# Optimization experiments

Measured on AMD Instinct MI355X. Metric: run time of the kernel, lower is better.

## Reference

```python
import jax, jax.numpy as jnp
import numpy as np

B, L, D, H = 2, 2048, 1024, 16
DH = D // H  # 64


def setup_inputs() -> dict:
    key = jax.random.key(0)
    ks = jax.random.split(key, 11)
    s = 0.02
    return {
        "src": jax.random.normal(ks[0], (B, L, D), dtype=jnp.float32),
        "Wq": jax.random.normal(ks[1], (D, D), dtype=jnp.float32) * s,
        "bq": jax.random.normal(ks[2], (D,), dtype=jnp.float32) * s,
        "Wk": jax.random.normal(ks[3], (D, D), dtype=jnp.float32) * s,
        "bk": jax.random.normal(ks[4], (D,), dtype=jnp.float32) * s,
        "Wv": jax.random.normal(ks[5], (D, D), dtype=jnp.float32) * s,
        "bv": jax.random.normal(ks[6], (D,), dtype=jnp.float32) * s,
        "Wo": jax.random.normal(ks[7], (D, D), dtype=jnp.float32) * s,
        "bo": jax.random.normal(ks[8], (D,), dtype=jnp.float32) * s,
        "conv_w": jax.random.normal(ks[9], (H, D, 3), dtype=jnp.float32) * s,  # Conv1d weight [out=H, in=D, k=3]
        "conv_b": jax.random.normal(ks[10], (H,), dtype=jnp.float32) * s,
    }


def reference(src, Wq, bq, Wk, bk, Wv, bv, Wo, bo, conv_w, conv_b):
    b, l, d = src.shape
    h, dh = H, DH
    # QKV projections (torch Linear: x @ W.T + b), split into heads: [B,H,L,DH]
    Q = (src @ Wq.T + bq).reshape(b, l, h, dh).transpose(0, 2, 1, 3)
    K = (src @ Wk.T + bk).reshape(b, l, h, dh).transpose(0, 2, 1, 3)
    V = (src @ Wv.T + bv).reshape(b, l, h, dh).transpose(0, 2, 1, 3)
    # saliency conv: Conv1d(D->H, k=3, padding='same') on [B,D,L] -> [B,H,L]
    sal = jax.lax.conv_general_dilated(
        src.transpose(0, 2, 1), conv_w,
        window_strides=(1,), padding=[(1, 1)],
        dimension_numbers=("NCH", "OIH", "NCH"),
    ) + conv_b[None, :, None]
    # attention scores + per-head saliency bias (broadcast over query axis)
    scores = jnp.einsum("bhqd,bhkd->bhqk", Q, K) / jnp.sqrt(jnp.float32(dh))
    scores = scores + sal[:, :, None, :]
    attn = jax.nn.softmax(scores, axis=-1)  # dropout is identity in eval
    out = jnp.einsum("bhqk,bhkd->bhqd", attn, V)  # [B,H,L,DH]
    out = out.transpose(0, 2, 1, 3).reshape(b, l, d)
    out = out @ Wo.T + bo
    return out, attn
```

## Files before the change

### kernel.cpp

```cpp
#include <hip/hip_runtime.h>

typedef __bf16 bf16x8 __attribute__((ext_vector_type(8)));
typedef float f32x4 __attribute__((ext_vector_type(4)));
typedef unsigned short u16;
typedef unsigned int u32;

#define MFMA(a, b, c) __builtin_amdgcn_mfma_f32_16x16x32_bf16((a), (b), (c), 0, 0, 0)


__device__ __forceinline__ u16 f2bf(float f) {
  u32 u = __float_as_uint(f);
  return (u16)((u + 0x7fffu + ((u >> 16) & 1u)) >> 16);
}

__global__ __launch_bounds__(256) void prep_all(
    const float4* __restrict__ src, const float4* __restrict__ wq,
    const float4* __restrict__ wk, const float4* __restrict__ wv,
    const float4* __restrict__ wo, const float* __restrict__ cw,
    uint2* __restrict__ srcb, uint2* __restrict__ wqb, uint2* __restrict__ wkb,
    uint2* __restrict__ wvb, uint2* __restrict__ wob, float* __restrict__ cwT) {
  int bx = blockIdx.x;
  if (bx < 8192) {
    const float4* in;
    uint2* out;
    int base;
    if (bx < 4096) { in = src; out = srcb; base = 0; }
    else if (bx < 5120) { in = wq; out = wqb; base = 4096; }
    else if (bx < 6144) { in = wk; out = wkb; base = 5120; }
    else if (bx < 7168) { in = wv; out = wvb; base = 6144; }
    else { in = wo; out = wob; base = 7168; }
    int i = (bx - base) * 256 + threadIdx.x;
    float4 v = in[i];
    uint2 o;
    o.x = (u32)f2bf(v.x) | ((u32)f2bf(v.y) << 16);
    o.y = (u32)f2bf(v.z) | ((u32)f2bf(v.w) << 16);
    out[i] = o;
  } else {
    int i = (bx - 8192) * 256 + threadIdx.x;
    int h = i / 3072;
    int j = (i - h * 3072) >> 10;
    int d = i & 1023;
    cwT[i] = cw[(h * 1024 + d) * 3 + j];
  }
}

__global__ __launch_bounds__(256) void conv_sal_k(const float* __restrict__ src,
                                                  const float* __restrict__ cwT,
                                                  const float* __restrict__ cb,
                                                  float* __restrict__ sal) {
  __shared__ float part[4][16][17];
  const int t = threadIdx.x;
  const int h = t & 15;
  const int li = (t >> 4) & 3;
  const int dc = t >> 6;
  const int b = blockIdx.y;
  const int l = blockIdx.x * 4 + li;
  float4 acc = {0.f, 0.f, 0.f, 0.f};
#pragma unroll
  for (int j = 0; j < 3; j++) {
    int ls = l + j - 1;
    if (ls < 0 || ls >= 2048) continue;
    const float4* sp = (const float4*)(src + ((size_t)b * 2048 + ls) * 1024 + dc * 256);
    const float4* wp = (const float4*)(cwT + (h * 3 + j) * 1024 + dc * 256);
    for (int d = 0; d < 64; d++) {
      float4 a = sp[d], w = wp[d];
      acc.x += a.x * w.x;
      acc.y += a.y * w.y;
      acc.z += a.z * w.z;
      acc.w += a.w * w.w;
    }
  }
  part[dc][li][h] = (acc.x + acc.y) + (acc.z + acc.w);
  __syncthreads();
  if (dc == 0) {
    float s = cb[h] + ((part[0][li][h] + part[1][li][h]) + (part[2][li][h] + part[3][li][h]));
    sal[(b * 16 + h) * 2048 + l] = s;
  }
}

__device__ __forceinline__ void gemm_core(const u16* __restrict__ Xg, const u16* __restrict__ Wg,
                                          int mblk, int nblk, u16* smA, u16* smB,
                                          f32x4 acc[4][4]) {
  const int t = threadIdx.x;
  const int lane = t & 63, wid = t >> 6;
  const int cl = lane & 15, gp = lane >> 4;
  const int r0 = t >> 2, cc = (t & 3) * 8;
  const u16* gA0 = Xg + (size_t)(mblk + r0) * 1024 + cc;
  const u16* gB0 = Wg + (size_t)(nblk + r0) * 1024 + cc;
  u16* lA0 = smA + t * 8;
  u16* lB0 = smB + t * 8;
  const u16* rA = smA + ((wid >> 1) * 64 + cl) * 32 + gp * 8;
  const u16* rB = smB + ((wid & 1) * 64 + cl) * 32 + gp * 8;
  for (int k0 = 0; k0 < 1024; k0 += 32) {
    bf16x8 sa0 = *(const bf16x8*)(gA0 + k0);
    bf16x8 sa1 = *(const bf16x8*)(gA0 + 64 * 1024 + k0);
    bf16x8 sb0 = *(const bf16x8*)(gB0 + k0);
    bf16x8 sb1 = *(const bf16x8*)(gB0 + 64 * 1024 + k0);
    __syncthreads();
    *(bf16x8*)lA0 = sa0;
    *(bf16x8*)(lA0 + 2048) = sa1;
    *(bf16x8*)lB0 = sb0;
    *(bf16x8*)(lB0 + 2048) = sb1;
    __syncthreads();
    bf16x8 a[4], b[4];
#pragma unroll
    for (int i = 0; i < 4; i++) {
      a[i] = *(const bf16x8*)(rA + i * 512);
      b[i] = *(const bf16x8*)(rB + i * 512);
    }
#pragma unroll
    for (int tm = 0; tm < 4; tm++)
#pragma unroll
      for (int tn = 0; tn < 4; tn++) acc[tm][tn] = MFMA(a[tm], b[tn], acc[tm][tn]);
  }
}

__global__ __launch_bounds__(256) void qkv_gemm(
    const u16* __restrict__ Xb, const u16* __restrict__ Wqb, const u16* __restrict__ Wkb,
    const u16* __restrict__ Wvb, const float* __restrict__ bq, const float* __restrict__ bk,
    const float* __restrict__ bv, u16* __restrict__ Qb, u16* __restrict__ Kb,
    u16* __restrict__ Vt) {
  __shared__ __align__(16) u16 smA[4096], smB[4096];
  const int seg = blockIdx.x >> 3;
  const u16* __restrict__ W = (seg == 0) ? Wqb : (seg == 1) ? Wkb : Wvb;
  const float* __restrict__ bias = (seg == 0) ? bq : (seg == 1) ? bk : bv;
  const int lane = threadIdx.x & 63, wid = threadIdx.x >> 6;
  const int cl = lane & 15, gp = lane >> 4;
  const int mblk = blockIdx.y * 128, nblk = (blockIdx.x & 7) * 128;
  const int m0 = mblk + (wid >> 1) * 64;
  const int n0 = nblk + (wid & 1) * 64;
  f32x4 acc[4][4] = {};
  gemm_core(Xb, W, mblk, nblk, smA, smB, acc);
#pragma unroll
  for (int tn = 0; tn < 4; tn++) {
    int col = n0 + tn * 16 + cl;
    float bv_ = bias[col];
    int hh = col >> 6, dh = col & 63;
#pragma unroll
    for (int tm = 0; tm < 4; tm++) {
#pragma unroll
      for (int r = 0; r < 4; r++) {
        int row = m0 + tm * 16 + gp * 4 + r;
        u16 hv = f2bf(acc[tm][tn][r] + bv_);
        int bb = row >> 11, l = row & 2047;
        if (seg == 0)
          Qb[(((size_t)(bb * 16 + hh) * 2048 + l) << 6) + dh] = hv;
        else if (seg == 1)
          Kb[(((size_t)(bb * 16 + hh) * 2048 + l) << 6) + dh] = hv;
        else
          Vt[((size_t)(bb * 16 + hh) * 64 + dh) * 2048 + l] = hv;
      }
    }
  }
}

__global__ __launch_bounds__(256) void out_gemm(const u16* __restrict__ Xb,
                                                const u16* __restrict__ W,
                                                const float* __restrict__ bias,
                                                float* __restrict__ Y) {
  __shared__ __align__(16) u16 smA[4096], smB[4096];
  const int lane = threadIdx.x & 63, wid = threadIdx.x >> 6;
  const int cl = lane & 15, gp = lane >> 4;
  const int mblk = blockIdx.y * 128, nblk = blockIdx.x * 128;
  const int m0 = mblk + (wid >> 1) * 64;
  const int n0 = nblk + (wid & 1) * 64;
  f32x4 acc[4][4] = {};
  gemm_core(Xb, W, mblk, nblk, smA, smB, acc);
#pragma unroll
  for (int tn = 0; tn < 4; tn++) {
    int col = n0 + tn * 16 + cl;
    float bv_ = bias[col];
#pragma unroll
    for (int tm = 0; tm < 4; tm++)
#pragma unroll
      for (int r = 0; r < 4; r++) {
        int row = m0 + tm * 16 + gp * 4 + r;
        Y[(size_t)row * 1024 + col] = acc[tm][tn][r] + bv_;
      }
  }
}

__global__ __launch_bounds__(128, 6) void flash_fused(const u16* __restrict__ Qb,
                                                      const u16* __restrict__ Kb,
                                                      const u16* __restrict__ Vt,
                                                      const float* __restrict__ sal,
                                                      float* __restrict__ attn,
                                                      u16* __restrict__ Ob) {
  __shared__ __align__(16) u16 pbuf[2][16][72];
  const int bh = blockIdx.x;
  const int b = bh >> 4, h = bh & 15;
  const int lane = threadIdx.x & 63, wid = threadIdx.x >> 6;
  const int cl = lane & 15, gp = lane >> 4;
  const int q0 = blockIdx.y * 32 + wid * 16;
  const u16* Qh = Qb + (size_t)bh * 2048 * 64;
  const u16* Kh = Kb + (size_t)bh * 2048 * 64;
  const u16* Vh = Vt + (size_t)bh * 64 * 2048;
  const float* salh = sal + bh * 2048;
  bf16x8 aQ0 = *(const bf16x8*)(Qh + (size_t)(q0 + cl) * 64 + gp * 8);
  bf16x8 aQ1 = *(const bf16x8*)(Qh + (size_t)(q0 + cl) * 64 + 32 + gp * 8);

  float ml[4], ll[4];
#pragma unroll
  for (int r = 0; r < 4; r++) { ml[r] = -1e30f; ll[r] = 0.f; }
  for (int kb = 0; kb < 2048; kb += 64) {
    f32x4 st[4];
#pragma unroll
    for (int tn = 0; tn < 4; tn++) {
      const u16* kp = Kh + (size_t)(kb + tn * 16 + cl) * 64 + gp * 8;
      f32x4 s = {};
      s = MFMA(aQ0, *(const bf16x8*)kp, s);
      s = MFMA(aQ1, *(const bf16x8*)(kp + 32), s);
      st[tn] = s;
    }
#pragma unroll
    for (int tn = 0; tn < 4; tn++) {
      float sv = salh[kb + tn * 16 + cl];
#pragma unroll
      for (int r = 0; r < 4; r++) st[tn][r] = st[tn][r] * 0.125f + sv;
    }
#pragma unroll
    for (int r = 0; r < 4; r++) {
      float v = fmaxf(fmaxf(st[0][r], st[1][r]), fmaxf(st[2][r], st[3][r]));
      float mn = fmaxf(ml[r], v);
      float alpha = __expf(ml[r] - mn);
      ml[r] = mn;
      float s0 = __expf(st[0][r] - mn) + __expf(st[1][r] - mn) + __expf(st[2][r] - mn) +
                 __expf(st[3][r] - mn);
      ll[r] = ll[r] * alpha + s0;
    }
  }
  float m[4], il[4];
#pragma unroll
  for (int r = 0; r < 4; r++) {
    float mr = ml[r];
    mr = fmaxf(mr, __shfl_xor(mr, 1));
    mr = fmaxf(mr, __shfl_xor(mr, 2));
    mr = fmaxf(mr, __shfl_xor(mr, 4));
    mr = fmaxf(mr, __shfl_xor(mr, 8));
    float lr = ll[r] * __expf(ml[r] - mr);
    lr += __shfl_xor(lr, 1);
    lr += __shfl_xor(lr, 2);
    lr += __shfl_xor(lr, 4);
    lr += __shfl_xor(lr, 8);
    m[r] = mr;
    il[r] = 1.0f / lr;
  }

  f32x4 oacc[4] = {};
  float* arow = attn + (size_t)bh * 2048 * 2048;
  u16* pw = &pbuf[wid][0][0];
  for (int kb = 0; kb < 2048; kb += 64) {
    f32x4 st[4];
#pragma unroll
    for (int tn = 0; tn < 4; tn++) {
      const u16* kp = Kh + (size_t)(kb + tn * 16 + cl) * 64 + gp * 8;
      f32x4 s = {};
      s = MFMA(aQ0, *(const bf16x8*)kp, s);
      s = MFMA(aQ1, *(const bf16x8*)(kp + 32), s);
      st[tn] = s;
    }
#pragma unroll
    for (int tn = 0; tn < 4; tn++) {
      float sv = salh[kb + tn * 16 + cl];
#pragma unroll
      for (int r = 0; r < 4; r++) {
        float p = __expf(st[tn][r] * 0.125f + sv - m[r]);
        arow[(size_t)(q0 + gp * 4 + r) * 2048 + kb + tn * 16 + cl] = p * il[r];
        pw[(gp * 4 + r) * 72 + tn * 16 + cl] = f2bf(p);
      }
    }
    asm volatile("s_waitcnt lgkmcnt(0)" ::: "memory");
    __builtin_amdgcn_sched_barrier(0);
    bf16x8 aP0 = *(const bf16x8*)(pw + cl * 72 + gp * 8);
    bf16x8 aP1 = *(const bf16x8*)(pw + cl * 72 + 32 + gp * 8);
    asm volatile("" ::: "memory");
#pragma unroll
    for (int tn = 0; tn < 4; tn++) {
      const u16* vp = Vh + (size_t)(tn * 16 + cl) * 2048 + kb + gp * 8;
      oacc[tn] = MFMA(aP0, *(const bf16x8*)vp, oacc[tn]);
      oacc[tn] = MFMA(aP1, *(const bf16x8*)(vp + 32), oacc[tn]);
    }
  }
#pragma unroll
  for (int tn = 0; tn < 4; tn++) {
    int d = h * 64 + tn * 16 + cl;
#pragma unroll
    for (int r = 0; r < 4; r++) {
      int q = q0 + gp * 4 + r;
      Ob[((size_t)(b * 2048 + q)) * 1024 + d] = f2bf(oacc[tn][r] * il[r]);
    }
  }
}

extern "C" void kernel_launch(void* const* d_in, const int* in_sizes, int n_in,
                              void* d_out, int out_size, void* d_ws, size_t ws_size,
                              hipStream_t stream) {
  const float* src = (const float*)d_in[0];
  const float* Wq = (const float*)d_in[1];
  const float* bq = (const float*)d_in[2];
  const float* Wk = (const float*)d_in[3];
  const float* bk = (const float*)d_in[4];
  const float* Wv = (const float*)d_in[5];
  const float* bv = (const float*)d_in[6];
  const float* Wo = (const float*)d_in[7];
  const float* bo = (const float*)d_in[8];
  const float* cw = (const float*)d_in[9];
  const float* cb = (const float*)d_in[10];

  char* ws = (char*)d_ws;
  u16* srcb = (u16*)(ws + 0);
  u16* wqb = (u16*)(ws + 8388608);
  u16* wkb = (u16*)(ws + 10485760);
  u16* wvb = (u16*)(ws + 12582912);
  u16* wob = (u16*)(ws + 14680064);
  u16* Qb = (u16*)(ws + 16777216);
  u16* Kb = (u16*)(ws + 25165824);
  u16* Vt = (u16*)(ws + 33554432);
  u16* Ob = (u16*)(ws + 41943040);
  float* cwT = (float*)(ws + 50331648);
  float* sal = (float*)(ws + 50528256);

  float* outp = (float*)d_out;
  float* attn = (float*)d_out + 4194304;

  prep_all<<<8384, 256, 0, stream>>>((const float4*)src, (const float4*)Wq, (const float4*)Wk,
                                     (const float4*)Wv, (const float4*)Wo, cw,
                                     (uint2*)srcb, (uint2*)wqb, (uint2*)wkb, (uint2*)wvb,
                                     (uint2*)wob, cwT);
  conv_sal_k<<<dim3(512, 2), 256, 0, stream>>>(src, cwT, cb, sal);
  qkv_gemm<<<dim3(24, 32), 256, 0, stream>>>(srcb, wqb, wkb, wvb, bq, bk, bv, Qb, Kb, Vt);
  flash_fused<<<dim3(32, 64), 128, 0, stream>>>(Qb, Kb, Vt, sal, attn, Ob);
  out_gemm<<<dim3(8, 32), 256, 0, stream>>>(Ob, wob, bo, outp);
}
```

Baseline: 1.100 ms.

## Double-buffer K tile loads and grow flash blocks to four waves

Both attention passes now prefetch the next 64-key K tile into registers while the current one feeds the MFMAs, using ping-pong register buffers. V tiles and saliency values are loaded ahead of the softmax work, and pointer arithmetic for the attn rows is hoisted into per-row incremented pointers. Blocks go from 2 to 4 waves (64 queries each) with half the grid, so more waves share L2 locality on K/V. This raises register pressure (launch bounds 256,3), which may limit occupancy. The kernel stays bound by the 268MB fp32 attn write.

```diff
diff --git a/kernel.cpp b/kernel.cpp
--- a/kernel.cpp
+++ b/kernel.cpp
@@ -180,54 +180,111 @@
   }
 }
 
-__global__ __launch_bounds__(128, 6) void flash_fused(const u16* __restrict__ Qb,
+#define P1_BODY(CUR, NXT, KB)                                                         \
+  do {                                                                                \
+    _Pragma("unroll") for (int tn = 0; tn < 4; tn++) {                                \
+      NXT[2 * tn] = *(const bf16x8*)(kp + tn * 1024);                                 \
+      NXT[2 * tn + 1] = *(const bf16x8*)(kp + tn * 1024 + 32);                        \
+    }                                                                                 \
+    kp += 4096;                                                                       \
+    float sv[4];                                                                      \
+    _Pragma("unroll") for (int tn = 0; tn < 4; tn++) sv[tn] = sp2[(KB) + tn * 16];    \
+    f32x4 st[4];                                                                      \
+    _Pragma("unroll") for (int tn = 0; tn < 4; tn++) {                                \
+      f32x4 s = {};                                                                   \
+      s = MFMA(aQ0, CUR[2 * tn], s);                                                  \
+      s = MFMA(aQ1, CUR[2 * tn + 1], s);                                              \
+      st[tn] = s;                                                                     \
+    }                                                                                 \
+    _Pragma("unroll") for (int tn = 0; tn < 4; tn++)                                  \
+        _Pragma("unroll") for (int r = 0; r < 4; r++) st[tn][r] =                     \
+            st[tn][r] * 0.125f + sv[tn];                                              \
+    _Pragma("unroll") for (int r = 0; r < 4; r++) {                                   \
+      float v = fmaxf(fmaxf(st[0][r], st[1][r]), fmaxf(st[2][r], st[3][r]));          \
+      float mn = fmaxf(ml[r], v);                                                     \
+      float alpha = __expf(ml[r] - mn);                                               \
+      ml[r] = mn;                                                                     \
+      float s0 = __expf(st[0][r] - mn) + __expf(st[1][r] - mn) +                      \
+                 __expf(st[2][r] - mn) + __expf(st[3][r] - mn);                       \
+      ll[r] = ll[r] * alpha + s0;                                                     \
+    }                                                                                 \
+  } while (0)
+
+#define P2_BODY(CUR, NXT, KB)                                                         \
+  do {                                                                                \
+    _Pragma("unroll") for (int tn = 0; tn < 4; tn++) {                                \
+      NXT[2 * tn] = *(const bf16x8*)(kp + tn * 1024);                                 \
+      NXT[2 * tn + 1] = *(const bf16x8*)(kp + tn * 1024 + 32);                        \
+    }                                                                                 \
+    kp += 4096;                                                                       \
+    f32x4 st[4];                                                                      \
+    _Pragma("unroll") for (int tn = 0; tn < 4; tn++) {                                \
+      f32x4 s = {};                                                                   \
+      s = MFMA(aQ0, CUR[2 * tn], s);                                                  \
+      s = MFMA(aQ1, CUR[2 * tn + 1], s);                                              \
+      st[tn] = s;                                                                     \
+    }                                                                                 \
+    bf16x8 vc[8];                                                                     \
+    _Pragma("unroll") for (int tn = 0; tn < 4; tn++) {                                \
+      vc[2 * tn] = *(const bf16x8*)(vb + tn * 32768 + (KB));                          \
+      vc[2 * tn + 1] = *(const bf16x8*)(vb + tn * 32768 + (KB) + 32);                 \
+    }                                                                                 \
+    float sv[4];                                                                      \
+    _Pragma("unroll") for (int tn = 0; tn < 4; tn++) sv[tn] = sp2[(KB) + tn * 16];    \
+    _Pragma("unroll") for (int tn = 0; tn < 4; tn++) {                                \
+      _Pragma("unroll") for (int r = 0; r < 4; r++) {                                 \
+        float p = __expf(st[tn][r] * 0.125f + sv[tn] - m[r]);                         \
+        pr[r][tn * 16] = p * il[r];                                                   \
+        pw[(gp * 4 + r) * 72 + tn * 16 + cl] = f2bf(p);                               \
+      }                                                                               \
+    }                                                                                 \
+    _Pragma("unroll") for (int r = 0; r < 4; r++) pr[r] += 64;                        \
+    asm volatile("s_waitcnt lgkmcnt(0)" ::: "memory");                                \
+    __builtin_amdgcn_sched_barrier(0);                                                \
+    bf16x8 aP0 = *(const bf16x8*)(pw + cl * 72 + gp * 8);                             \
+    bf16x8 aP1 = *(const bf16x8*)(pw + cl * 72 + 32 + gp * 8);                        \
+    asm volatile("" ::: "memory");                                                    \
+    _Pragma("unroll") for (int tn = 0; tn < 4; tn++) {                                \
+      oacc[tn] = MFMA(aP0, vc[2 * tn], oacc[tn]);                                     \
+      oacc[tn] = MFMA(aP1, vc[2 * tn + 1], oacc[tn]);                                 \
+    }                                                                                 \
+  } while (0)
+
+__global__ __launch_bounds__(256, 3) void flash_fused(const u16* __restrict__ Qb,
                                                       const u16* __restrict__ Kb,
                                                       const u16* __restrict__ Vt,
                                                       const float* __restrict__ sal,
                                                       float* __restrict__ attn,
                                                       u16* __restrict__ Ob) {
-  __shared__ __align__(16) u16 pbuf[2][16][72];
+  __shared__ __align__(16) u16 pbuf[4][16][72];
   const int bh = blockIdx.x;
   const int b = bh >> 4, h = bh & 15;
   const int lane = threadIdx.x & 63, wid = threadIdx.x >> 6;
   const int cl = lane & 15, gp = lane >> 4;
-  const int q0 = blockIdx.y * 32 + wid * 16;
+  const int q0 = blockIdx.y * 64 + wid * 16;
   const u16* Qh = Qb + (size_t)bh * 2048 * 64;
   const u16* Kh = Kb + (size_t)bh * 2048 * 64;
   const u16* Vh = Vt + (size_t)bh * 64 * 2048;
-  const float* salh = sal + bh * 2048;
+  const float* sp2 = sal + bh * 2048 + cl;
   bf16x8 aQ0 = *(const bf16x8*)(Qh + (size_t)(q0 + cl) * 64 + gp * 8);
   bf16x8 aQ1 = *(const bf16x8*)(Qh + (size_t)(q0 + cl) * 64 + 32 + gp * 8);
+  const u16* kbase = Kh + cl * 64 + gp * 8;
+  const u16* vb = Vh + cl * 2048 + gp * 8;
 
   float ml[4], ll[4];
 #pragma unroll
   for (int r = 0; r < 4; r++) { ml[r] = -1e30f; ll[r] = 0.f; }
-  for (int kb = 0; kb < 2048; kb += 64) {
-    f32x4 st[4];
-#pragma unroll
-    for (int tn = 0; tn < 4; tn++) {
-      const u16* kp = Kh + (size_t)(kb + tn * 16 + cl) * 64 + gp * 8;
-      f32x4 s = {};
-      s = MFMA(aQ0, *(const bf16x8*)kp, s);
-      s = MFMA(aQ1, *(const bf16x8*)(kp + 32), s);
-      st[tn] = s;
-    }
-#pragma unroll
-    for (int tn = 0; tn < 4; tn++) {
-      float sv = salh[kb + tn * 16 + cl];
-#pragma unroll
-      for (int r = 0; r < 4; r++) st[tn][r] = st[tn][r] * 0.125f + sv;
-    }
-#pragma unroll
-    for (int r = 0; r < 4; r++) {
-      float v = fmaxf(fmaxf(st[0][r], st[1][r]), fmaxf(st[2][r], st[3][r]));
-      float mn = fmaxf(ml[r], v);
-      float alpha = __expf(ml[r] - mn);
-      ml[r] = mn;
-      float s0 = __expf(st[0][r] - mn) + __expf(st[1][r] - mn) + __expf(st[2][r] - mn) +
-                 __expf(st[3][r] - mn);
-      ll[r] = ll[r] * alpha + s0;
-    }
+  bf16x8 ka[8], kbg[8];
+  const u16* kp = kbase;
+#pragma unroll
+  for (int tn = 0; tn < 4; tn++) {
+    ka[2 * tn] = *(const bf16x8*)(kp + tn * 1024);
+    ka[2 * tn + 1] = *(const bf16x8*)(kp + tn * 1024 + 32);
+  }
+  kp += 4096;
+  for (int kb = 0; kb < 2048; kb += 128) {
+    P1_BODY(ka, kbg, kb);
+    P1_BODY(kbg, ka, kb + 64);
   }
   float m[4], il[4];
 #pragma unroll
@@ -247,39 +304,21 @@
   }
 
   f32x4 oacc[4] = {};
-  float* arow = attn + (size_t)bh * 2048 * 2048;
+  float* pr[4];
+#pragma unroll
+  for (int r = 0; r < 4; r++)
+    pr[r] = attn + (size_t)bh * 2048 * 2048 + (size_t)(q0 + gp * 4 + r) * 2048 + cl;
   u16* pw = &pbuf[wid][0][0];
-  for (int kb = 0; kb < 2048; kb += 64) {
-    f32x4 st[4];
-#pragma unroll
-    for (int tn = 0; tn < 4; tn++) {
-      const u16* kp = Kh + (size_t)(kb + tn * 16 + cl) * 64 + gp * 8;
-      f32x4 s = {};
-      s = MFMA(aQ0, *(const bf16x8*)kp, s);
-      s = MFMA(aQ1, *(const bf16x8*)(kp + 32), s);
-      st[tn] = s;
-    }
-#pragma unroll
-    for (int tn = 0; tn < 4; tn++) {
-      float sv = salh[kb + tn * 16 + cl];
-#pragma unroll
-      for (int r = 0; r < 4; r++) {
-        float p = __expf(st[tn][r] * 0.125f + sv - m[r]);
-        arow[(size_t)(q0 + gp * 4 + r) * 2048 + kb + tn * 16 + cl] = p * il[r];
-        pw[(gp * 4 + r) * 72 + tn * 16 + cl] = f2bf(p);
-      }
-    }
-    asm volatile("s_waitcnt lgkmcnt(0)" ::: "memory");
-    __builtin_amdgcn_sched_barrier(0);
-    bf16x8 aP0 = *(const bf16x8*)(pw + cl * 72 + gp * 8);
-    bf16x8 aP1 = *(const bf16x8*)(pw + cl * 72 + 32 + gp * 8);
-    asm volatile("" ::: "memory");
-#pragma unroll
-    for (int tn = 0; tn < 4; tn++) {
-      const u16* vp = Vh + (size_t)(tn * 16 + cl) * 2048 + kb + gp * 8;
-      oacc[tn] = MFMA(aP0, *(const bf16x8*)vp, oacc[tn]);
-      oacc[tn] = MFMA(aP1, *(const bf16x8*)(vp + 32), oacc[tn]);
-    }
+  kp = kbase;
+#pragma unroll
+  for (int tn = 0; tn < 4; tn++) {
+    ka[2 * tn] = *(const bf16x8*)(kp + tn * 1024);
+    ka[2 * tn + 1] = *(const bf16x8*)(kp + tn * 1024 + 32);
+  }
+  kp += 4096;
+  for (int kb = 0; kb < 2048; kb += 128) {
+    P2_BODY(ka, kbg, kb);
+    P2_BODY(kbg, ka, kb + 64);
   }
 #pragma unroll
   for (int tn = 0; tn < 4; tn++) {
@@ -329,6 +368,6 @@
                                      (uint2*)wob, cwT);
   conv_sal_k<<<dim3(512, 2), 256, 0, stream>>>(src, cwT, cb, sal);
   qkv_gemm<<<dim3(24, 32), 256, 0, stream>>>(srcb, wqb, wkb, wvb, bq, bk, bv, Qb, Kb, Vt);
-  flash_fused<<<dim3(32, 64), 128, 0, stream>>>(Qb, Kb, Vt, sal, attn, Ob);
+  flash_fused<<<dim3(32, 32), 256, 0, stream>>>(Qb, Kb, Vt, sal, attn, Ob);
   out_gemm<<<dim3(8, 32), 256, 0, stream>>>(Ob, wob, bo, outp);
 }
```

New measurement: 1.056 ms. 1.04x faster.
